# Optimization experiments

Hardware: AMD Instinct MI355X
Metric: run time of the kernel (lower is better)

## Reference

```python
import jax, jax.numpy as jnp
import numpy as np


def _haar_kernel():
    # 8 orthonormal 3D Haar taps, order (zf,yf,xf) in {L,H}^3 -> subband index s=4*z+2*y+x
    s2 = np.sqrt(2.0)
    L = np.array([1.0, 1.0]) / s2
    H = np.array([1.0, -1.0]) / s2
    taps = []
    for zf in (L, H):
        for yf in (L, H):
            for xf in (L, H):
                taps.append(np.einsum('i,j,k->ijk', zf, yf, xf))
    return jnp.asarray(np.stack(taps, 0), dtype=jnp.float32)  # [8,2,2,2]


def setup_inputs() -> dict:
    key = jax.random.key(0)
    ks = jax.random.split(key, 9)
    C, mid = 128, 8  # channels=128, reduction=16 -> mid = max(1, 128//16)
    x = jax.random.normal(ks[0], (2, C, 64, 64, 64), jnp.float32)
    def p(k, shape):
        return jax.random.normal(k, shape, jnp.float32) * 0.05
    return {
        'x': x,
        'gw1': p(ks[1], (mid, C)), 'gb1': p(ks[2], (mid,)),
        'gw2': p(ks[3], (C, mid)), 'gb2': p(ks[4], (C,)),
        'lw1': p(ks[5], (mid, C)), 'lb1': p(ks[6], (mid,)),
        'lw2': p(ks[7], (C, mid)), 'lb2': p(ks[8], (C,)),
    }


def _mlp(t, w1, b1, w2, b2):
    # 1x1x1 Conv3d -> ReLU -> 1x1x1 Conv3d, t: [B,C,D,H,W]
    h = jnp.einsum('bcdhw,mc->bmdhw', t, w1) + b1[None, :, None, None, None]
    h = jax.nn.relu(h)
    return jnp.einsum('bmdhw,cm->bcdhw', h, w2) + b2[None, :, None, None, None]


def reference(x, gw1, gb1, gw2, gb2, lw1, lb1, lw2, lb2):
    k = _haar_kernel()  # [8,2,2,2]
    B, C, D, H, W = x.shape
    # depthwise stride-2 2x2x2 conv == non-overlapping block transform
    xr = x.reshape(B, C, D // 2, 2, H // 2, 2, W // 2, 2)
    y = jnp.einsum('bcdphqwr,spqr->bcsdhw', xr, k)  # [B,C,8,D/2,H/2,W/2]
    low = y[:, :, 0]        # [B,C,D/2,H/2,W/2]
    highs = y[:, :, 1:]     # [B,C,7,D/2,H/2,W/2]
    x_sum = low + highs.sum(axis=2)
    gap = x_sum.mean(axis=(2, 3, 4), keepdims=True)  # AdaptiveAvgPool3d(1)
    w = jax.nn.sigmoid(_mlp(gap, gw1, gb1, gw2, gb2) + _mlp(x_sum, lw1, lb1, lw2, lb2))
    y_mod = jnp.concatenate([low[:, :, None], highs * w[:, :, None]], axis=2)
    # conv_transpose of orthonormal Haar == inverse block transform
    xr2 = jnp.einsum('bcsdhw,spqr->bcdphqwr', y_mod, k)
    return xr2.reshape(B, C, D, H, W)
```

## Files before the change

kernel.cpp:

```cpp
#include <hip/hip_runtime.h>
#include <math.h>

#define C_ 128
#define MID 8
#define CS 262144
static __device__ __forceinline__ float sigmoidf_(float z) {
    return 1.0f / (1.0f + __expf(-z));
}
#define SQRT8 2.8284271247461903f

__global__ __launch_bounds__(256) void gap_kernel(const float* __restrict__ x,
                                                  float* __restrict__ gap) {
    const int bc = blockIdx.x;
    const float* xb = x + (size_t)bc * CS;
    float s = 0.0f;
    for (int j = threadIdx.x; j < 32768; j += 256) {
        int d  = j >> 10;
        int h  = (j >> 5) & 31;
        int f2 = j & 31;
        const float2* row = (const float2*)(xb + (size_t)(((2 * d) * 64 + 2 * h) * 64));
        s += row[f2].x;
    }
    __shared__ float red[256];
    red[threadIdx.x] = s;
    __syncthreads();
    for (int off = 128; off > 0; off >>= 1) {
        if (threadIdx.x < off) red[threadIdx.x] += red[threadIdx.x + off];
        __syncthreads();
    }
    if (threadIdx.x == 0) gap[bc] = red[0] * (SQRT8 / 32768.0f);
}

__global__ __launch_bounds__(256) void gmlp_kernel(const float* __restrict__ gap,
                                                   const float* __restrict__ gw1,
                                                   const float* __restrict__ gb1,
                                                   const float* __restrict__ gw2,
                                                   const float* __restrict__ gb2,
                                                   float* __restrict__ gout) {
    __shared__ float hid[2][MID];
    const int t = threadIdx.x;
    if (t < 2 * MID) {
        int b = t >> 3, m = t & 7;
        float a = gb1[m];
        for (int c = 0; c < C_; ++c) a += gw1[m * C_ + c] * gap[b * C_ + c];
        hid[b][m] = fmaxf(a, 0.0f);
    }
    __syncthreads();
    int b = t >> 7, c = t & 127;
    float a = gb2[c];
    for (int m = 0; m < MID; ++m) a += gw2[c * MID + m] * hid[b][m];
    gout[t] = a;
}

__global__ __launch_bounds__(256) void main_kernel(const float* __restrict__ x,
                                                   const float* __restrict__ lw1,
                                                   const float* __restrict__ lb1,
                                                   const float* __restrict__ lw2,
                                                   const float* __restrict__ lb2,
                                                   const float* __restrict__ gout,
                                                   float* __restrict__ out) {
    __shared__ float xs[C_ * 32];
    __shared__ float hid[MID * 32];
    __shared__ float slw1[MID * C_];
    __shared__ float slw2[C_ * MID];
    __shared__ float slb1[MID];
    __shared__ float slb2[C_];
    __shared__ float sgout[C_];

    const int blk = blockIdx.x;
    const int b  = blk >> 10;
    const int dc = (blk >> 5) & 31;
    const int hc = blk & 31;
    const int tid = threadIdx.x;

    for (int i = tid; i < MID * C_; i += 256) slw1[i] = lw1[i];
    for (int i = tid; i < C_ * MID; i += 256) slw2[i] = lw2[i];
    if (tid < MID) slb1[tid] = lb1[tid];
    if (tid < C_) { slb2[tid] = lb2[tid]; sgout[tid] = gout[b * C_ + tid]; }

    const float* xb = x + (size_t)b * C_ * CS;
    float* ob = out + (size_t)b * C_ * CS;
    const int rowoff = ((2 * dc) * 64 + 2 * hc) * 64;

    {
        int c = tid >> 5, f2 = tid & 31;
        for (int it = 0; it < 16; ++it, c += 8) {
            const float2* row = (const float2*)(xb + (size_t)c * CS + rowoff);
            xs[c * 32 + f2] = SQRT8 * row[f2].x;
        }
    }
    __syncthreads();

    {
        int m = tid >> 5, wc = tid & 31;
        float a = slb1[m];
        for (int c = 0; c < C_; ++c) a += slw1[m * C_ + c] * xs[c * 32 + wc];
        hid[m * 32 + wc] = fmaxf(a, 0.0f);
    }
    __syncthreads();

    {
        int wc = tid & 31, c0 = tid >> 5;
        float hv[MID];
        for (int m = 0; m < MID; ++m) hv[m] = hid[m * 32 + wc];
        for (int i = 0; i < 16; ++i) {
            int c = c0 * 16 + i;
            float a = slb2[c] + sgout[c];
            for (int m = 0; m < MID; ++m) a += slw2[c * MID + m] * hv[m];
            xs[c * 32 + wc] = sigmoidf_(a);
        }
    }
    __syncthreads();

    {
        int wc = tid & 31, cg = tid >> 5;
        for (int it = 0; it < 16; ++it) {
            int c = cg + 8 * it;
            const float* base = xb + (size_t)c * CS + rowoff;
            float* obase = ob + (size_t)c * CS + rowoff;
            float2 a00 = ((const float2*)(base))[wc];
            float2 a01 = ((const float2*)(base + 64))[wc];
            float2 a10 = ((const float2*)(base + 4096))[wc];
            float2 a11 = ((const float2*)(base + 4096 + 64))[wc];
            float mean = (a00.x + a00.y + a01.x + a01.y +
                          a10.x + a10.y + a11.x + a11.y) * 0.125f;
            float wv = xs[c * 32 + wc];
            float om = (1.0f - wv) * mean;
            float2 o;
            o.x = wv * a00.x + om; o.y = wv * a00.y + om; ((float2*)(obase))[wc] = o;
            o.x = wv * a01.x + om; o.y = wv * a01.y + om; ((float2*)(obase + 64))[wc] = o;
            o.x = wv * a10.x + om; o.y = wv * a10.y + om; ((float2*)(obase + 4096))[wc] = o;
            o.x = wv * a11.x + om; o.y = wv * a11.y + om; ((float2*)(obase + 4096 + 64))[wc] = o;
        }
    }
}

extern "C" void kernel_launch(void* const* d_in, const int* in_sizes, int n_in,
                              void* d_out, int out_size, void* d_ws, size_t ws_size,
                              hipStream_t stream) {
    const float* x   = (const float*)d_in[0];
    const float* gw1 = (const float*)d_in[1];
    const float* gb1 = (const float*)d_in[2];
    const float* gw2 = (const float*)d_in[3];
    const float* gb2 = (const float*)d_in[4];
    const float* lw1 = (const float*)d_in[5];
    const float* lb1 = (const float*)d_in[6];
    const float* lw2 = (const float*)d_in[7];
    const float* lb2 = (const float*)d_in[8];
    float* o  = (float*)d_out;
    float* ws = (float*)d_ws;

    gap_kernel<<<256, 256, 0, stream>>>(x, ws);
    gmlp_kernel<<<1, 256, 0, stream>>>(ws, gw1, gb1, gw2, gb2, ws + 256);
    main_kernel<<<2048, 256, 0, stream>>>(x, lw1, lb1, lw2, lb2, ws + 256, o);
}
```

Before: 524.8 us.

## Fuse GAP into corner MLP kernel and split blend into separate coalesced kernel

After: 489.8 us. 6.7% less time.

```diff
diff --git a/kernel.cpp b/kernel.cpp
--- a/kernel.cpp
+++ b/kernel.cpp
@@ -4,68 +4,23 @@
 #define C_ 128
 #define MID 8
 #define CS 262144
+#define SQRT8 2.8284271247461903f
+
 static __device__ __forceinline__ float sigmoidf_(float z) {
     return 1.0f / (1.0f + __expf(-z));
 }
-#define SQRT8 2.8284271247461903f
 
-__global__ __launch_bounds__(256) void gap_kernel(const float* __restrict__ x,
-                                                  float* __restrict__ gap) {
-    const int bc = blockIdx.x;
-    const float* xb = x + (size_t)bc * CS;
-    float s = 0.0f;
-    for (int j = threadIdx.x; j < 32768; j += 256) {
-        int d  = j >> 10;
-        int h  = (j >> 5) & 31;
-        int f2 = j & 31;
-        const float2* row = (const float2*)(xb + (size_t)(((2 * d) * 64 + 2 * h) * 64));
-        s += row[f2].x;
-    }
-    __shared__ float red[256];
-    red[threadIdx.x] = s;
-    __syncthreads();
-    for (int off = 128; off > 0; off >>= 1) {
-        if (threadIdx.x < off) red[threadIdx.x] += red[threadIdx.x + off];
-        __syncthreads();
-    }
-    if (threadIdx.x == 0) gap[bc] = red[0] * (SQRT8 / 32768.0f);
-}
-
-__global__ __launch_bounds__(256) void gmlp_kernel(const float* __restrict__ gap,
-                                                   const float* __restrict__ gw1,
-                                                   const float* __restrict__ gb1,
-                                                   const float* __restrict__ gw2,
-                                                   const float* __restrict__ gb2,
-                                                   float* __restrict__ gout) {
-    __shared__ float hid[2][MID];
-    const int t = threadIdx.x;
-    if (t < 2 * MID) {
-        int b = t >> 3, m = t & 7;
-        float a = gb1[m];
-        for (int c = 0; c < C_; ++c) a += gw1[m * C_ + c] * gap[b * C_ + c];
-        hid[b][m] = fmaxf(a, 0.0f);
-    }
-    __syncthreads();
-    int b = t >> 7, c = t & 127;
-    float a = gb2[c];
-    for (int m = 0; m < MID; ++m) a += gw2[c * MID + m] * hid[b][m];
-    gout[t] = a;
-}
-
-__global__ __launch_bounds__(256) void main_kernel(const float* __restrict__ x,
-                                                   const float* __restrict__ lw1,
-                                                   const float* __restrict__ lb1,
-                                                   const float* __restrict__ lw2,
-                                                   const float* __restrict__ lb2,
-                                                   const float* __restrict__ gout,
-                                                   float* __restrict__ out) {
-    __shared__ float xs[C_ * 32];
+__global__ __launch_bounds__(256) void corner_kernel(
+    const float* __restrict__ x,
+    const float* __restrict__ lw1, const float* __restrict__ lb1,
+    const float* __restrict__ lw2, const float* __restrict__ lb2,
+    float* __restrict__ partial,
+    float* __restrict__ lout)
+{
+    __shared__ float xs[C_ * 33];
     __shared__ float hid[MID * 32];
     __shared__ float slw1[MID * C_];
     __shared__ float slw2[C_ * MID];
-    __shared__ float slb1[MID];
-    __shared__ float slb2[C_];
-    __shared__ float sgout[C_];
 
     const int blk = blockIdx.x;
     const int b  = blk >> 10;
@@ -75,26 +30,30 @@
 
     for (int i = tid; i < MID * C_; i += 256) slw1[i] = lw1[i];
     for (int i = tid; i < C_ * MID; i += 256) slw2[i] = lw2[i];
-    if (tid < MID) slb1[tid] = lb1[tid];
-    if (tid < C_) { slb2[tid] = lb2[tid]; sgout[tid] = gout[b * C_ + tid]; }
 
-    const float* xb = x + (size_t)b * C_ * CS;
-    float* ob = out + (size_t)b * C_ * CS;
-    const int rowoff = ((2 * dc) * 64 + 2 * hc) * 64;
-
+    const float* xb = x + (size_t)b * C_ * CS + (size_t)(((2 * dc) * 64 + 2 * hc) * 64);
+    const int f = tid & 15;
     {
-        int c = tid >> 5, f2 = tid & 31;
-        for (int it = 0; it < 16; ++it, c += 8) {
-            const float2* row = (const float2*)(xb + (size_t)c * CS + rowoff);
-            xs[c * 32 + f2] = SQRT8 * row[f2].x;
+        int c = tid >> 4;
+        #pragma unroll
+        for (int k = 0; k < 8; ++k, c += 16) {
+            float4 v = ((const float4*)(xb + (size_t)c * CS))[f];
+            xs[c * 33 + 2 * f]     = SQRT8 * v.x;
+            xs[c * 33 + 2 * f + 1] = SQRT8 * v.z;
+            float sc = v.x + v.z;
+            sc += __shfl_down(sc, 8);
+            sc += __shfl_down(sc, 4);
+            sc += __shfl_down(sc, 2);
+            sc += __shfl_down(sc, 1);
+            if (f == 0) partial[blk * C_ + c] = sc;
         }
     }
     __syncthreads();
 
     {
         int m = tid >> 5, wc = tid & 31;
-        float a = slb1[m];
-        for (int c = 0; c < C_; ++c) a += slw1[m * C_ + c] * xs[c * 32 + wc];
+        float a = lb1[m];
+        for (int cc = 0; cc < C_; ++cc) a += slw1[m * C_ + cc] * xs[cc * 33 + wc];
         hid[m * 32 + wc] = fmaxf(a, 0.0f);
     }
     __syncthreads();
@@ -102,37 +61,105 @@
     {
         int wc = tid & 31, c0 = tid >> 5;
         float hv[MID];
+        #pragma unroll
         for (int m = 0; m < MID; ++m) hv[m] = hid[m * 32 + wc];
+        float* lo = lout + (size_t)blk * (C_ * 32);
+        #pragma unroll
         for (int i = 0; i < 16; ++i) {
-            int c = c0 * 16 + i;
-            float a = slb2[c] + sgout[c];
-            for (int m = 0; m < MID; ++m) a += slw2[c * MID + m] * hv[m];
-            xs[c * 32 + wc] = sigmoidf_(a);
+            int cc = c0 * 16 + i;
+            float a = lb2[cc];
+            #pragma unroll
+            for (int m = 0; m < MID; ++m) a += slw2[cc * MID + m] * hv[m];
+            lo[cc * 32 + wc] = a;
         }
     }
+}
+
+__global__ __launch_bounds__(1024) void gmlp_kernel(
+    const float* __restrict__ partial,
+    const float* __restrict__ gw1, const float* __restrict__ gb1,
+    const float* __restrict__ gw2, const float* __restrict__ gb2,
+    float* __restrict__ gout)
+{
+    __shared__ float red[8][C_];
+    __shared__ float sgap[C_];
+    __shared__ float shid[MID];
+    const int b = blockIdx.x;
+    const int t = threadIdx.x;
+    const int c = t & 127, chunk = t >> 7;
+    float s = 0.0f;
+    const float* p = partial + (size_t)(b * 1024 + chunk * 128) * C_ + c;
+    for (int j = 0; j < 128; ++j) s += p[(size_t)j * C_];
+    red[chunk][c] = s;
     __syncthreads();
+    if (t < C_) {
+        float tot = 0.0f;
+        #pragma unroll
+        for (int k = 0; k < 8; ++k) tot += red[k][c];
+        sgap[c] = tot * (SQRT8 / 32768.0f);
+    }
+    __syncthreads();
+    if (t < MID) {
+        float a = gb1[t];
+        for (int cc = 0; cc < C_; ++cc) a += gw1[t * C_ + cc] * sgap[cc];
+        shid[t] = fmaxf(a, 0.0f);
+    }
+    __syncthreads();
+    if (t < C_) {
+        float a = gb2[t];
+        #pragma unroll
+        for (int m = 0; m < MID; ++m) a += gw2[t * MID + m] * shid[m];
+        gout[b * C_ + t] = a;
+    }
+}
 
-    {
-        int wc = tid & 31, cg = tid >> 5;
-        for (int it = 0; it < 16; ++it) {
-            int c = cg + 8 * it;
-            const float* base = xb + (size_t)c * CS + rowoff;
-            float* obase = ob + (size_t)c * CS + rowoff;
-            float2 a00 = ((const float2*)(base))[wc];
-            float2 a01 = ((const float2*)(base + 64))[wc];
-            float2 a10 = ((const float2*)(base + 4096))[wc];
-            float2 a11 = ((const float2*)(base + 4096 + 64))[wc];
-            float mean = (a00.x + a00.y + a01.x + a01.y +
-                          a10.x + a10.y + a11.x + a11.y) * 0.125f;
-            float wv = xs[c * 32 + wc];
-            float om = (1.0f - wv) * mean;
-            float2 o;
-            o.x = wv * a00.x + om; o.y = wv * a00.y + om; ((float2*)(obase))[wc] = o;
-            o.x = wv * a01.x + om; o.y = wv * a01.y + om; ((float2*)(obase + 64))[wc] = o;
-            o.x = wv * a10.x + om; o.y = wv * a10.y + om; ((float2*)(obase + 4096))[wc] = o;
-            o.x = wv * a11.x + om; o.y = wv * a11.y + om; ((float2*)(obase + 4096 + 64))[wc] = o;
-        }
-    }
+__global__ __launch_bounds__(256) void blend_kernel(
+    const float* __restrict__ x,
+    const float* __restrict__ lout,
+    const float* __restrict__ gout,
+    float* __restrict__ out)
+{
+    const int blk  = blockIdx.x;
+    const int half = blk & 1;
+    const int dc   = (blk >> 1) & 31;
+    const int c    = (blk >> 6) & 127;
+    const int b    = blk >> 13;
+    const int tid  = threadIdx.x;
+    const int f    = tid & 15;
+    const int hc   = half * 16 + (tid >> 4);
+
+    const size_t off = (size_t)(b * C_ + c) * CS
+                     + (size_t)(2 * dc) * 4096 + (size_t)(2 * hc) * 64;
+    float4 a00 = ((const float4*)(x + off))[f];
+    float4 a01 = ((const float4*)(x + off + 64))[f];
+    float4 a10 = ((const float4*)(x + off + 4096))[f];
+    float4 a11 = ((const float4*)(x + off + 4160))[f];
+
+    const float go = gout[b * C_ + c];
+    const float2 g2 = *(const float2*)(lout
+        + ((size_t)(((b * 32 + dc) * 32 + hc) * C_ + c)) * 32 + 2 * f);
+    const float w0 = sigmoidf_(g2.x + go);
+    const float w1 = sigmoidf_(g2.y + go);
+    const float mean0 = (a00.x + a00.y + a01.x + a01.y +
+                         a10.x + a10.y + a11.x + a11.y) * 0.125f;
+    const float mean1 = (a00.z + a00.w + a01.z + a01.w +
+                         a10.z + a10.w + a11.z + a11.w) * 0.125f;
+    const float om0 = (1.0f - w0) * mean0;
+    const float om1 = (1.0f - w1) * mean1;
+
+    float4 o;
+    o.x = w0 * a00.x + om0; o.y = w0 * a00.y + om0;
+    o.z = w1 * a00.z + om1; o.w = w1 * a00.w + om1;
+    ((float4*)(out + off))[f] = o;
+    o.x = w0 * a01.x + om0; o.y = w0 * a01.y + om0;
+    o.z = w1 * a01.z + om1; o.w = w1 * a01.w + om1;
+    ((float4*)(out + off + 64))[f] = o;
+    o.x = w0 * a10.x + om0; o.y = w0 * a10.y + om0;
+    o.z = w1 * a10.z + om1; o.w = w1 * a10.w + om1;
+    ((float4*)(out + off + 4096))[f] = o;
+    o.x = w0 * a11.x + om0; o.y = w0 * a11.y + om0;
+    o.z = w1 * a11.z + om1; o.w = w1 * a11.w + om1;
+    ((float4*)(out + off + 4160))[f] = o;
 }
 
 extern "C" void kernel_launch(void* const* d_in, const int* in_sizes, int n_in,
@@ -150,7 +177,11 @@
     float* o  = (float*)d_out;
     float* ws = (float*)d_ws;
 
-    gap_kernel<<<256, 256, 0, stream>>>(x, ws);
-    gmlp_kernel<<<1, 256, 0, stream>>>(ws, gw1, gb1, gw2, gb2, ws + 256);
-    main_kernel<<<2048, 256, 0, stream>>>(x, lw1, lb1, lw2, lb2, ws + 256, o);
+    float* partial = ws;
+    float* gout    = ws + 262144;
+    float* lout    = ws + 262400;
+
+    corner_kernel<<<2048, 256, 0, stream>>>(x, lw1, lb1, lw2, lb2, partial, lout);
+    gmlp_kernel<<<2, 1024, 0, stream>>>(partial, gw1, gb1, gw2, gb2, gout);
+    blend_kernel<<<16384, 256, 0, stream>>>(x, lout, gout, o);
 }
```
